# Kernel tuning notes

Measured on AMD Instinct MI355X. Metric: run time of the kernel, lower is better.

The kernel has to match this reference:

```python
import jax, jax.numpy as jnp
import numpy as np

D = 1024
H = 16
DH = D // H
FF = 4096
EPS = 1e-6


def setup_inputs() -> dict:
    key = jax.random.key(0)
    ks = jax.random.split(key, 8)
    s = 1.0 / np.sqrt(D)
    return {
        "x": jax.random.normal(ks[0], (2, 2048, D), jnp.float32),
        # attention projections stored [in, out] (math equals torch Linear x @ W.T)
        "w_q": jax.random.normal(ks[1], (D, D), jnp.float32) * s,
        "w_k": jax.random.normal(ks[2], (D, D), jnp.float32) * s,
        "w_v": jax.random.normal(ks[3], (D, D), jnp.float32) * s,
        "w_o": jax.random.normal(ks[4], (D, D), jnp.float32) * s,
        "w1": jax.random.normal(ks[5], (D, FF), jnp.float32) * s,
        "b1": jnp.zeros((FF,), jnp.float32),
        "w2": jax.random.normal(ks[6], (FF, D), jnp.float32) * (1.0 / np.sqrt(FF)),
        "b2": jnp.zeros((D,), jnp.float32),
        "g1": jnp.ones((D,), jnp.float32),
        "be1": jnp.zeros((D,), jnp.float32),
        "g2": jnp.ones((D,), jnp.float32),
        "be2": jnp.zeros((D,), jnp.float32),
    }


def _layernorm(x, gamma, beta):
    # torch .std() uses Bessel correction (ddof=1); note std+eps, not var+eps
    mean = jnp.mean(x, axis=-1, keepdims=True)
    std = jnp.std(x, axis=-1, keepdims=True, ddof=1)
    return gamma * (x - mean) / (std + EPS) + beta


def _attention(h, w_q, w_k, w_v, w_o):
    B, S, _ = h.shape
    q = (h @ w_q).reshape(B, S, H, DH)
    k = (h @ w_k).reshape(B, S, H, DH)
    v = (h @ w_v).reshape(B, S, H, DH)
    scores = jnp.einsum('bqhd,bkhd->bhqk', q, k) / np.sqrt(DH)  # [B,H,S,S]
    attn = jax.nn.softmax(scores, axis=-1)
    out = jnp.einsum('bhqk,bkhd->bqhd', attn, v).reshape(B, S, D)
    return out @ w_o


def reference(x, w_q, w_k, w_v, w_o, w1, b1, w2, b2, g1, be1, g2, be2):
    # pre-norm residual 1: self-attention (dropout=0 / eval)
    x = x + _attention(_layernorm(x, g1, be1), w_q, w_k, w_v, w_o)
    # pre-norm residual 2: FFN
    h = _layernorm(x, g2, be2)
    x = x + (jax.nn.relu(h @ w1 + b1) @ w2 + b2)
    return x
```

## Files before the change

kernel.cpp:

```cpp
#include <hip/hip_runtime.h>


typedef _Float16 half8 __attribute__((ext_vector_type(8)));
typedef _Float16 half4 __attribute__((ext_vector_type(4)));
typedef __fp16 fp16x2 __attribute__((ext_vector_type(2)));
typedef float floatx4 __attribute__((ext_vector_type(4)));

__device__ __forceinline__ void async16(const void* g, void* l) {
    __builtin_amdgcn_global_load_lds((const __attribute__((address_space(1))) unsigned int*)g,
                                     (__attribute__((address_space(3))) unsigned int*)l,
                                     16, 0, 0);
}

__global__ __launch_bounds__(256) void ln_kernel(const float* __restrict__ x,
                                                 const float* __restrict__ g,
                                                 const float* __restrict__ be,
                                                 _Float16* __restrict__ out) {
    int row = blockIdx.x;
    int tid = threadIdx.x;
    floatx4 v = ((const floatx4*)(x + (size_t)row * 1024))[tid];
    float s = 0.f, ss = 0.f;
#pragma unroll
    for (int i = 0; i < 4; i++) { s += v[i]; ss += v[i] * v[i]; }
#pragma unroll
    for (int off = 1; off < 64; off <<= 1) {
        s += __shfl_xor(s, off);
        ss += __shfl_xor(ss, off);
    }
    __shared__ float sm[8];
    int wave = tid >> 6, lane = tid & 63;
    if (lane == 0) { sm[wave] = s; sm[wave + 4] = ss; }
    __syncthreads();
    s = sm[0] + sm[1] + sm[2] + sm[3];
    ss = sm[4] + sm[5] + sm[6] + sm[7];
    float mean = s * (1.f / 1024.f);
    float var = (ss - s * mean) * (1.f / 1023.f);
    float rs = 1.f / (sqrtf(fmaxf(var, 0.f)) + 1e-6f);
    floatx4 gv = ((const floatx4*)g)[tid];
    floatx4 bv = ((const floatx4*)be)[tid];
    half4 o;
#pragma unroll
    for (int i = 0; i < 4; i++) o[i] = (_Float16)(gv[i] * (v[i] - mean) * rs + bv[i]);
    ((half4*)(out + (size_t)row * 1024))[tid] = o;
}

__global__ __launch_bounds__(256) void convt_kernel(const float* __restrict__ W, int ldW,
                                                    _Float16* __restrict__ WT, int Kr,
                                                    float scale) {
    __shared__ float t[64][65];
    int n0 = blockIdx.x * 64, k0 = blockIdx.y * 64;
    int tid = threadIdx.x;
    int r = tid >> 4, c4 = (tid & 15) * 4;
#pragma unroll
    for (int p = 0; p < 4; p++) {
        floatx4 v = *(const floatx4*)(W + (size_t)(k0 + r + p * 16) * ldW + n0 + c4);
#pragma unroll
        for (int j = 0; j < 4; j++) t[c4 + j][r + p * 16] = v[j];
    }
    __syncthreads();
#pragma unroll
    for (int p = 0; p < 4; p++) {
        int rr = r + p * 16;
        half4 o;
#pragma unroll
        for (int j = 0; j < 4; j++) o[j] = (_Float16)(t[rr][c4 + j] * scale);
        *(half4*)(WT + (size_t)(n0 + rr) * Kr + k0 + c4) = o;
    }
}

__global__ __launch_bounds__(256) void transv_kernel(const _Float16* __restrict__ V, int ldv,
                                                     _Float16* __restrict__ Vt) {
    __shared__ _Float16 t[64][72];
    int t0 = blockIdx.x * 64, d0 = blockIdx.y * 64;
    int tid = threadIdx.x;
#pragma unroll
    for (int i = 0; i < 2; i++) {
        int v = tid + i * 256;
        int r = v >> 3, c = (v & 7) * 8;
        half8 vv = *(const half8*)(V + (size_t)(t0 + r) * ldv + d0 + c);
#pragma unroll
        for (int j = 0; j < 8; j++) t[c + j][r] = vv[j];
    }
    __syncthreads();
    int bh = (t0 >> 11) * 16 + (d0 >> 6);
    int sbase = t0 & 2047;
#pragma unroll
    for (int i = 0; i < 2; i++) {
        int v = tid + i * 256;
        int r = v >> 3, c = (v & 7) * 8;
        half8 o = *(const half8*)&t[r][c];
        *(half8*)(Vt + ((size_t)bh * 64 + r) * 2048 + sbase + c) = o;
    }
}

__global__ __launch_bounds__(256) void gemm_t(const _Float16* __restrict__ A, int lda,
                                              const _Float16* __restrict__ BT,
                                              const float* __restrict__ bias,
                                              const float* res, void* Cout,
                                              int N, int K, int relu_flag, int out_fp16) {
    __shared__ _Float16 As[64 * 64];
    __shared__ _Float16 Bs[128 * 64];
    int tid = threadIdx.x;
    int wave = tid >> 6, lane = tid & 63, quad = lane >> 4, l15 = lane & 15;
    int bm = blockIdx.y * 64, bn = blockIdx.x * 128;
    int wr = (wave & 1) * 32, wc = (wave >> 1) * 64;
    int lrow = lane >> 3, lch = lane & 7;

    floatx4 acc[2][4];
#pragma unroll
    for (int im = 0; im < 2; im++)
#pragma unroll
        for (int in = 0; in < 4; in++)
#pragma unroll
            for (int r = 0; r < 4; r++) acc[im][in][r] = 0.f;

    for (int k0 = 0; k0 < K; k0 += 64) {
        __syncthreads();
#pragma unroll
        for (int ia = 0; ia < 2; ia++) {
            int g = 2 * wave + ia;
            int row = g * 8 + lrow;
            int ch = lch ^ (row & 7);
            async16(A + (size_t)(bm + row) * lda + k0 + ch * 8, &As[g * 512]);
        }
#pragma unroll
        for (int ib = 0; ib < 4; ib++) {
            int g = 4 * wave + ib;
            int row = g * 8 + lrow;
            int ch = lch ^ (row & 7);
            async16(BT + (size_t)(bn + row) * K + k0 + ch * 8, &Bs[g * 512]);
        }
        __syncthreads();

        half8 af[2][2], bf[4][2];
#pragma unroll
        for (int kk = 0; kk < 2; kk++) {
#pragma unroll
            for (int im = 0; im < 2; im++) {
                int m = wr + im * 16 + l15;
                af[im][kk] = *(const half8*)&As[m * 64 + ((((kk << 2) | quad) ^ (m & 7)) << 3)];
            }
#pragma unroll
            for (int in = 0; in < 4; in++) {
                int n = wc + in * 16 + l15;
                bf[in][kk] = *(const half8*)&Bs[n * 64 + ((((kk << 2) | quad) ^ (n & 7)) << 3)];
            }
        }
#pragma unroll
        for (int kk = 0; kk < 2; kk++)
#pragma unroll
            for (int im = 0; im < 2; im++)
#pragma unroll
                for (int in = 0; in < 4; in++)
                    acc[im][in] = __builtin_amdgcn_mfma_f32_16x16x32_f16(af[im][kk], bf[in][kk],
                                                                         acc[im][in], 0, 0, 0);
    }
#pragma unroll
    for (int im = 0; im < 2; im++)
#pragma unroll
        for (int in = 0; in < 4; in++)
#pragma unroll
            for (int r = 0; r < 4; r++) {
                int row = bm + wr + im * 16 + quad * 4 + r;
                int col = bn + wc + in * 16 + l15;
                float val = acc[im][in][r];
                if (bias) val += bias[col];
                if (relu_flag) val = fmaxf(val, 0.f);
                if (res) val += res[(size_t)row * N + col];
                if (out_fp16) ((_Float16*)Cout)[(size_t)row * N + col] = (_Float16)val;
                else          ((float*)Cout)[(size_t)row * N + col] = val;
            }
}

template <int BUF>
__device__ __forceinline__ void attn_step(const half8* const (&kfp)[2][4][2],
                                          const half4* const (&vfp)[2][4][4],
                                          const half8 (&bq)[2],
                                          floatx4 (&o_acc)[4],
                                          float& m_i, float& l_i) {
    const float LOG2E = 1.44269504f;
    floatx4 s_acc[4];
#pragma unroll
    for (int jn = 0; jn < 4; jn++)
#pragma unroll
        for (int r = 0; r < 4; r++) s_acc[jn][r] = 0.f;
#pragma unroll
    for (int jn = 0; jn < 4; jn++)
#pragma unroll
        for (int kk = 0; kk < 2; kk++)
            s_acc[jn] = __builtin_amdgcn_mfma_f32_16x16x32_f16(*kfp[BUF][jn][kk], bq[kk],
                                                               s_acc[jn], 0, 0, 0);

    float mx = -1e30f;
#pragma unroll
    for (int jn = 0; jn < 4; jn++)
#pragma unroll
        for (int r = 0; r < 4; r++) mx = fmaxf(mx, s_acc[jn][r]);
    mx = fmaxf(mx, __shfl_xor(mx, 16));
    mx = fmaxf(mx, __shfl_xor(mx, 32));
    if (!__all(mx <= m_i + 8.f)) {
        float mnew = fmaxf(m_i, mx);
        float dd = m_i - mnew;
        float alpha = (dd < -60.f) ? 0.f : __expf(dd);
        l_i *= alpha;
#pragma unroll
        for (int im = 0; im < 4; im++)
#pragma unroll
            for (int r = 0; r < 4; r++) o_acc[im][r] *= alpha;
        m_i = mnew;
    }
    float m2 = m_i * LOG2E;

    float sum = 0.f;
    half4 pb[4];
#pragma unroll
    for (int jn = 0; jn < 4; jn++) {
        float p0 = exp2f(fmaf(s_acc[jn][0], LOG2E, -m2));
        float p1 = exp2f(fmaf(s_acc[jn][1], LOG2E, -m2));
        float p2 = exp2f(fmaf(s_acc[jn][2], LOG2E, -m2));
        float p3 = exp2f(fmaf(s_acc[jn][3], LOG2E, -m2));
        sum += (p0 + p1) + (p2 + p3);
        fp16x2 lo = __builtin_amdgcn_cvt_pkrtz(p0, p1);
        fp16x2 hi = __builtin_amdgcn_cvt_pkrtz(p2, p3);
        pb[jn][0] = (_Float16)lo[0]; pb[jn][1] = (_Float16)lo[1];
        pb[jn][2] = (_Float16)hi[0]; pb[jn][3] = (_Float16)hi[1];
    }
    sum += __shfl_xor(sum, 16);
    sum += __shfl_xor(sum, 32);
    l_i += sum;

#pragma unroll
    for (int im = 0; im < 4; im++)
#pragma unroll
        for (int ks = 0; ks < 4; ks++)
            o_acc[im] = __builtin_amdgcn_mfma_f32_16x16x16f16(*vfp[BUF][im][ks], pb[ks],
                                                              o_acc[im], 0, 0, 0);
}

__global__ __launch_bounds__(256) void attn_kernel(const _Float16* Q,
                                                   const _Float16* __restrict__ K,
                                                   const _Float16* __restrict__ Vt,
                                                   _Float16* O, int ld) {
    __shared__ _Float16 Qs[64 * 64];
    __shared__ _Float16 KVs[2][2][64 * 64];
    int qt = blockIdx.x, bh = blockIdx.y;
    int b = bh >> 4, h = bh & 15;
    int col0 = h * 64, tbase = b * 2048;
    int tid = threadIdx.x;
    int wave = tid >> 6, lane = tid & 63, quad = lane >> 4, l15 = lane & 15;
    int lrow = lane >> 3, lch = lane & 7;

    const _Float16* kg[2];
    const _Float16* vg[2];
    const size_t kadv = (size_t)64 * ld;
#pragma unroll
    for (int i = 0; i < 2; i++) {
        int g = 2 * wave + i;
        int row = g * 8 + lrow;
        int ch = lch ^ (row & 7);
        kg[i] = K + (size_t)(tbase + row) * ld + col0 + ch * 8;
        vg[i] = Vt + ((size_t)bh * 64 + row) * 2048 + ch * 8;
        async16(Q + (size_t)(tbase + qt * 64 + row) * ld + col0 + ch * 8, &Qs[g * 512]);
        async16(kg[i], &KVs[0][0][g * 512]);
        async16(vg[i], &KVs[0][1][g * 512]);
        kg[i] += kadv;
        vg[i] += 64;
    }
    __syncthreads();

    int rowq = 16 * wave + l15;
    half8 bq[2];
#pragma unroll
    for (int kk = 0; kk < 2; kk++)
        bq[kk] = *(const half8*)&Qs[rowq * 64 + ((((kk << 2) | quad) ^ (rowq & 7)) << 3)];

    const half8* kfp[2][4][2];
    const half4* vfp[2][4][4];
#pragma unroll
    for (int bb = 0; bb < 2; bb++) {
#pragma unroll
        for (int jn = 0; jn < 4; jn++) {
            int rowk = 16 * jn + l15;
#pragma unroll
            for (int kk = 0; kk < 2; kk++)
                kfp[bb][jn][kk] = (const half8*)
                    &KVs[bb][0][rowk * 64 + ((((kk << 2) | quad) ^ (rowk & 7)) << 3)];
        }
#pragma unroll
        for (int im = 0; im < 4; im++) {
            int rowv = 16 * im + l15;
#pragma unroll
            for (int ks = 0; ks < 4; ks++) {
                int off = rowv * 128 + ((((2 * ks) | (quad >> 1)) ^ (rowv & 7)) << 4)
                          + (quad & 1) * 8;
                vfp[bb][im][ks] = (const half4*)((const char*)KVs[bb][1] + off);
            }
        }
    }

    floatx4 o_acc[4];
#pragma unroll
    for (int im = 0; im < 4; im++)
#pragma unroll
        for (int r = 0; r < 4; r++) o_acc[im][r] = 0.f;
    float m_i = -1e30f, l_i = 0.f;

#pragma unroll 1
    for (int kt2 = 0; kt2 < 16; kt2++) {
        if (kt2) __syncthreads();
#pragma unroll
        for (int i = 0; i < 2; i++) {
            async16(kg[i], &KVs[1][0][(2 * wave + i) * 512]);
            async16(vg[i], &KVs[1][1][(2 * wave + i) * 512]);
            kg[i] += kadv;
            vg[i] += 64;
        }
        attn_step<0>(kfp, vfp, bq, o_acc, m_i, l_i);

        __syncthreads();
        if (kt2 < 15) {
#pragma unroll
            for (int i = 0; i < 2; i++) {
                async16(kg[i], &KVs[0][0][(2 * wave + i) * 512]);
                async16(vg[i], &KVs[0][1][(2 * wave + i) * 512]);
                kg[i] += kadv;
                vg[i] += 64;
            }
        }
        attn_step<1>(kfp, vfp, bq, o_acc, m_i, l_i);
    }

    float rl = 1.f / l_i;
#pragma unroll
    for (int im = 0; im < 4; im++) {
        half4 o;
#pragma unroll
        for (int r = 0; r < 4; r++) o[r] = (_Float16)(o_acc[im][r] * rl);
        *(half4*)&O[(size_t)(tbase + qt * 64 + wave * 16 + l15) * ld + col0 + im * 16 + quad * 4] = o;
    }
}

extern "C" void kernel_launch(void* const* d_in, const int* in_sizes, int n_in,
                              void* d_out, int out_size, void* d_ws, size_t ws_size,
                              hipStream_t stream) {
    const float* x   = (const float*)d_in[0];
    const float* wq  = (const float*)d_in[1];
    const float* wk  = (const float*)d_in[2];
    const float* wv  = (const float*)d_in[3];
    const float* wo  = (const float*)d_in[4];
    const float* w1  = (const float*)d_in[5];
    const float* b1  = (const float*)d_in[6];
    const float* w2  = (const float*)d_in[7];
    const float* b2  = (const float*)d_in[8];
    const float* g1  = (const float*)d_in[9];
    const float* be1 = (const float*)d_in[10];
    const float* g2  = (const float*)d_in[11];
    const float* be2 = (const float*)d_in[12];

    const size_t M1 = (size_t)1 << 20;
    _Float16* R0  = (_Float16*)d_ws;
    _Float16* QKV = R0 + 4 * M1;
    _Float16* R3  = R0 + 12 * M1;

    _Float16* wqkvT = (_Float16*)d_out;
    float* x1 = (float*)d_out;
    float* out = (float*)d_out;

    dim3 blk(256);

    convt_kernel<<<dim3(16, 16), blk, 0, stream>>>(wq, 1024, wqkvT, 1024, 0.125f);
    convt_kernel<<<dim3(16, 16), blk, 0, stream>>>(wk, 1024, wqkvT + (size_t)1024 * 1024, 1024, 1.f);
    convt_kernel<<<dim3(16, 16), blk, 0, stream>>>(wv, 1024, wqkvT + (size_t)2048 * 1024, 1024, 1.f);
    ln_kernel<<<4096, blk, 0, stream>>>(x, g1, be1, R0);
    gemm_t<<<dim3(24, 64), blk, 0, stream>>>(R0, 1024, wqkvT, nullptr, nullptr, QKV, 3072, 1024, 0, 1);
    transv_kernel<<<dim3(64, 16), blk, 0, stream>>>(QKV + 2048, 3072, R0);
    attn_kernel<<<dim3(32, 32), blk, 0, stream>>>(QKV, QKV + 1024, R0, QKV, 3072);
    convt_kernel<<<dim3(16, 16), blk, 0, stream>>>(wo, 1024, R0, 1024, 1.f);
    gemm_t<<<dim3(8, 64), blk, 0, stream>>>(QKV, 3072, R0, nullptr, x, x1, 1024, 1024, 0, 0);
    ln_kernel<<<4096, blk, 0, stream>>>(x1, g2, be2, R0);
    _Float16* f = QKV;
    for (int hh = 0; hh < 2; hh++) {
        _Float16* w1Th = R3;
        _Float16* w2Th = R3 + 2 * M1;
        convt_kernel<<<dim3(32, 16), blk, 0, stream>>>(w1 + hh * 2048, 4096, w1Th, 1024, 1.f);
        gemm_t<<<dim3(16, 64), blk, 0, stream>>>(R0, 1024, w1Th, b1 + hh * 2048, nullptr, f,
                                                 2048, 1024, 1, 1);
        convt_kernel<<<dim3(16, 32), blk, 0, stream>>>(w2 + (size_t)hh * 2048 * 1024, 1024, w2Th, 2048, 1.f);
        gemm_t<<<dim3(8, 64), blk, 0, stream>>>(f, 2048, w2Th, (hh == 1) ? b2 : nullptr, x1, out,
                                                1024, 2048, 0, 0);
    }
}
```

Measured before the change: 465.3 us.

## Merge weight-conversion launches, add 128x128 GEMM tile for QKV, tighten softmax reductions

The three Q/K/V weight transpose-convert launches become one grid-z kernel, and each FFN half's w1/w2 conversions become one paired launch, so fewer kernels are launched. A new 128x128-tile GEMM with a 4x4 MFMA fragment per wave is used for the QKV projection to raise data reuse per block. In attention, the row-max uses a three-input max tree and the probability sum uses independent partial sums to shorten dependency chains. The larger tile uses more registers and LDS and halves the QKV grid, which may lower occupancy.

Measured after the change: 442.2 us. 1.05x faster.

```diff
diff --git a/kernel.cpp b/kernel.cpp
--- a/kernel.cpp
+++ b/kernel.cpp
@@ -5,6 +5,8 @@
 typedef _Float16 half4 __attribute__((ext_vector_type(4)));
 typedef __fp16 fp16x2 __attribute__((ext_vector_type(2)));
 typedef float floatx4 __attribute__((ext_vector_type(4)));
+
+#define MAX3(a, b, c) fmaxf(fmaxf((a), (b)), (c))
 
 __device__ __forceinline__ void async16(const void* g, void* l) {
     __builtin_amdgcn_global_load_lds((const __attribute__((address_space(1))) unsigned int*)g,
@@ -44,28 +46,60 @@
     ((half4*)(out + (size_t)row * 1024))[tid] = o;
 }
 
+__device__ __forceinline__ void convt_body(const float* __restrict__ W, int ldW,
+                                           _Float16* __restrict__ WT, int Kr, float scale,
+                                           int n0, int k0) {
+    __shared__ float t[64][65];
+    int tid = threadIdx.x;
+    int r = tid >> 4, c4 = (tid & 15) * 4;
+#pragma unroll
+    for (int p = 0; p < 4; p++) {
+        floatx4 v = *(const floatx4*)(W + (size_t)(k0 + r + p * 16) * ldW + n0 + c4);
+#pragma unroll
+        for (int j = 0; j < 4; j++) t[c4 + j][r + p * 16] = v[j];
+    }
+    __syncthreads();
+#pragma unroll
+    for (int p = 0; p < 4; p++) {
+        int rr = r + p * 16;
+        half4 o;
+#pragma unroll
+        for (int j = 0; j < 4; j++) o[j] = (_Float16)(t[rr][c4 + j] * scale);
+        *(half4*)(WT + (size_t)(n0 + rr) * Kr + k0 + c4) = o;
+    }
+}
+
 __global__ __launch_bounds__(256) void convt_kernel(const float* __restrict__ W, int ldW,
                                                     _Float16* __restrict__ WT, int Kr,
                                                     float scale) {
-    __shared__ float t[64][65];
-    int n0 = blockIdx.x * 64, k0 = blockIdx.y * 64;
-    int tid = threadIdx.x;
-    int r = tid >> 4, c4 = (tid & 15) * 4;
-#pragma unroll
-    for (int p = 0; p < 4; p++) {
-        floatx4 v = *(const floatx4*)(W + (size_t)(k0 + r + p * 16) * ldW + n0 + c4);
-#pragma unroll
-        for (int j = 0; j < 4; j++) t[c4 + j][r + p * 16] = v[j];
-    }
-    __syncthreads();
-#pragma unroll
-    for (int p = 0; p < 4; p++) {
-        int rr = r + p * 16;
-        half4 o;
-#pragma unroll
-        for (int j = 0; j < 4; j++) o[j] = (_Float16)(t[rr][c4 + j] * scale);
-        *(half4*)(WT + (size_t)(n0 + rr) * Kr + k0 + c4) = o;
-    }
+    convt_body(W, ldW, WT, Kr, scale, blockIdx.x * 64, blockIdx.y * 64);
+}
+
+__global__ __launch_bounds__(256) void convt3_kernel(const float* __restrict__ W0,
+                                                     const float* __restrict__ W1,
+                                                     const float* __restrict__ W2,
+                                                     _Float16* __restrict__ QT) {
+    int z = blockIdx.z;
+    const float* W = (z == 0) ? W0 : (z == 1) ? W1 : W2;
+    _Float16* WT = QT + (size_t)z * 1024 * 1024;
+    float scale = (z == 0) ? 0.125f : 1.f;
+    convt_body(W, 1024, WT, 1024, scale, blockIdx.x * 64, blockIdx.y * 64);
+}
+
+__global__ __launch_bounds__(256) void convt_pair_kernel(const float* __restrict__ Wa, int ldWa,
+                                                         _Float16* __restrict__ WTa, int Kra,
+                                                         int gxa, int gya,
+                                                         const float* __restrict__ Wb, int ldWb,
+                                                         _Float16* __restrict__ WTb, int Krb,
+                                                         int gxb, int gyb) {
+    int z = blockIdx.z;
+    const float* W = z ? Wb : Wa;
+    _Float16* WT = z ? WTb : WTa;
+    int ldW = z ? ldWb : ldWa;
+    int Kr = z ? Krb : Kra;
+    int gx = z ? gxb : gxa, gy = z ? gyb : gya;
+    if ((int)blockIdx.x >= gx || (int)blockIdx.y >= gy) return;
+    convt_body(W, ldW, WT, Kr, 1.f, blockIdx.x * 64, blockIdx.y * 64);
 }
 
 __global__ __launch_bounds__(256) void transv_kernel(const _Float16* __restrict__ V, int ldv,
@@ -172,6 +206,85 @@
             }
 }
 
+__global__ __launch_bounds__(256) void gemm_t128(const _Float16* __restrict__ A, int lda,
+                                                 const _Float16* __restrict__ BT,
+                                                 const float* __restrict__ bias,
+                                                 const float* res, void* Cout,
+                                                 int N, int K, int relu_flag, int out_fp16) {
+    __shared__ _Float16 As[128 * 64];
+    __shared__ _Float16 Bs[128 * 64];
+    int tid = threadIdx.x;
+    int wave = tid >> 6, lane = tid & 63, quad = lane >> 4, l15 = lane & 15;
+    int bm = blockIdx.y * 128, bn = blockIdx.x * 128;
+    int wr = (wave & 1) * 64, wc = (wave >> 1) * 64;
+    int lrow = lane >> 3, lch = lane & 7;
+
+    floatx4 acc[4][4];
+#pragma unroll
+    for (int im = 0; im < 4; im++)
+#pragma unroll
+        for (int in = 0; in < 4; in++)
+#pragma unroll
+            for (int r = 0; r < 4; r++) acc[im][in][r] = 0.f;
+
+    for (int k0 = 0; k0 < K; k0 += 64) {
+        __syncthreads();
+#pragma unroll
+        for (int ia = 0; ia < 4; ia++) {
+            int g = 4 * wave + ia;
+            int row = g * 8 + lrow;
+            int ch = lch ^ (row & 7);
+            async16(A + (size_t)(bm + row) * lda + k0 + ch * 8, &As[g * 512]);
+        }
+#pragma unroll
+        for (int ib = 0; ib < 4; ib++) {
+            int g = 4 * wave + ib;
+            int row = g * 8 + lrow;
+            int ch = lch ^ (row & 7);
+            async16(BT + (size_t)(bn + row) * K + k0 + ch * 8, &Bs[g * 512]);
+        }
+        __syncthreads();
+
+        half8 af[4][2], bf[4][2];
+#pragma unroll
+        for (int kk = 0; kk < 2; kk++) {
+#pragma unroll
+            for (int im = 0; im < 4; im++) {
+                int m = wr + im * 16 + l15;
+                af[im][kk] = *(const half8*)&As[m * 64 + ((((kk << 2) | quad) ^ (m & 7)) << 3)];
+            }
+#pragma unroll
+            for (int in = 0; in < 4; in++) {
+                int n = wc + in * 16 + l15;
+                bf[in][kk] = *(const half8*)&Bs[n * 64 + ((((kk << 2) | quad) ^ (n & 7)) << 3)];
+            }
+        }
+#pragma unroll
+        for (int kk = 0; kk < 2; kk++)
+#pragma unroll
+            for (int im = 0; im < 4; im++)
+#pragma unroll
+                for (int in = 0; in < 4; in++)
+                    acc[im][in] = __builtin_amdgcn_mfma_f32_16x16x32_f16(af[im][kk], bf[in][kk],
+                                                                         acc[im][in], 0, 0, 0);
+    }
+#pragma unroll
+    for (int im = 0; im < 4; im++)
+#pragma unroll
+        for (int in = 0; in < 4; in++)
+#pragma unroll
+            for (int r = 0; r < 4; r++) {
+                int row = bm + wr + im * 16 + quad * 4 + r;
+                int col = bn + wc + in * 16 + l15;
+                float val = acc[im][in][r];
+                if (bias) val += bias[col];
+                if (relu_flag) val = fmaxf(val, 0.f);
+                if (res) val += res[(size_t)row * N + col];
+                if (out_fp16) ((_Float16*)Cout)[(size_t)row * N + col] = (_Float16)val;
+                else          ((float*)Cout)[(size_t)row * N + col] = val;
+            }
+}
+
 template <int BUF>
 __device__ __forceinline__ void attn_step(const half8* const (&kfp)[2][4][2],
                                           const half4* const (&vfp)[2][4][4],
@@ -191,11 +304,12 @@
             s_acc[jn] = __builtin_amdgcn_mfma_f32_16x16x32_f16(*kfp[BUF][jn][kk], bq[kk],
                                                                s_acc[jn], 0, 0, 0);
 
-    float mx = -1e30f;
-#pragma unroll
-    for (int jn = 0; jn < 4; jn++)
-#pragma unroll
-        for (int r = 0; r < 4; r++) mx = fmaxf(mx, s_acc[jn][r]);
+    float t0 = MAX3(s_acc[0][0], s_acc[0][1], s_acc[0][2]);
+    float t1 = MAX3(s_acc[0][3], s_acc[1][0], s_acc[1][1]);
+    float t2 = MAX3(s_acc[1][2], s_acc[1][3], s_acc[2][0]);
+    float t3 = MAX3(s_acc[2][1], s_acc[2][2], s_acc[2][3]);
+    float t4 = MAX3(s_acc[3][0], s_acc[3][1], s_acc[3][2]);
+    float mx = MAX3(MAX3(t0, t1, t2), fmaxf(t3, t4), s_acc[3][3]);
     mx = fmaxf(mx, __shfl_xor(mx, 16));
     mx = fmaxf(mx, __shfl_xor(mx, 32));
     if (!__all(mx <= m_i + 8.f)) {
@@ -211,7 +325,7 @@
     }
     float m2 = m_i * LOG2E;
 
-    float sum = 0.f;
+    float sj[4];
     half4 pb[4];
 #pragma unroll
     for (int jn = 0; jn < 4; jn++) {
@@ -219,12 +333,13 @@
         float p1 = exp2f(fmaf(s_acc[jn][1], LOG2E, -m2));
         float p2 = exp2f(fmaf(s_acc[jn][2], LOG2E, -m2));
         float p3 = exp2f(fmaf(s_acc[jn][3], LOG2E, -m2));
-        sum += (p0 + p1) + (p2 + p3);
+        sj[jn] = (p0 + p1) + (p2 + p3);
         fp16x2 lo = __builtin_amdgcn_cvt_pkrtz(p0, p1);
         fp16x2 hi = __builtin_amdgcn_cvt_pkrtz(p2, p3);
         pb[jn][0] = (_Float16)lo[0]; pb[jn][1] = (_Float16)lo[1];
         pb[jn][2] = (_Float16)hi[0]; pb[jn][3] = (_Float16)hi[1];
     }
+    float sum = (sj[0] + sj[1]) + (sj[2] + sj[3]);
     sum += __shfl_xor(sum, 16);
     sum += __shfl_xor(sum, 32);
     l_i += sum;
@@ -368,24 +483,24 @@
 
     dim3 blk(256);
 
-    convt_kernel<<<dim3(16, 16), blk, 0, stream>>>(wq, 1024, wqkvT, 1024, 0.125f);
-    convt_kernel<<<dim3(16, 16), blk, 0, stream>>>(wk, 1024, wqkvT + (size_t)1024 * 1024, 1024, 1.f);
-    convt_kernel<<<dim3(16, 16), blk, 0, stream>>>(wv, 1024, wqkvT + (size_t)2048 * 1024, 1024, 1.f);
+    convt3_kernel<<<dim3(16, 16, 3), blk, 0, stream>>>(wq, wk, wv, wqkvT);
     ln_kernel<<<4096, blk, 0, stream>>>(x, g1, be1, R0);
-    gemm_t<<<dim3(24, 64), blk, 0, stream>>>(R0, 1024, wqkvT, nullptr, nullptr, QKV, 3072, 1024, 0, 1);
+    gemm_t128<<<dim3(24, 32), blk, 0, stream>>>(R0, 1024, wqkvT, nullptr, nullptr, QKV, 3072, 1024, 0, 1);
     transv_kernel<<<dim3(64, 16), blk, 0, stream>>>(QKV + 2048, 3072, R0);
     attn_kernel<<<dim3(32, 32), blk, 0, stream>>>(QKV, QKV + 1024, R0, QKV, 3072);
-    convt_kernel<<<dim3(16, 16), blk, 0, stream>>>(wo, 1024, R0, 1024, 1.f);
-    gemm_t<<<dim3(8, 64), blk, 0, stream>>>(QKV, 3072, R0, nullptr, x, x1, 1024, 1024, 0, 0);
+    _Float16* woT = R0;
+    convt_kernel<<<dim3(16, 16), blk, 0, stream>>>(wo, 1024, woT, 1024, 1.f);
+    gemm_t<<<dim3(8, 64), blk, 0, stream>>>(QKV, 3072, woT, nullptr, x, x1, 1024, 1024, 0, 0);
     ln_kernel<<<4096, blk, 0, stream>>>(x1, g2, be2, R0);
     _Float16* f = QKV;
     for (int hh = 0; hh < 2; hh++) {
         _Float16* w1Th = R3;
         _Float16* w2Th = R3 + 2 * M1;
-        convt_kernel<<<dim3(32, 16), blk, 0, stream>>>(w1 + hh * 2048, 4096, w1Th, 1024, 1.f);
+        convt_pair_kernel<<<dim3(32, 32, 2), blk, 0, stream>>>(
+            w1 + hh * 2048, 4096, w1Th, 1024, 32, 16,
+            w2 + (size_t)hh * 2048 * 1024, 1024, w2Th, 2048, 16, 32);
         gemm_t<<<dim3(16, 64), blk, 0, stream>>>(R0, 1024, w1Th, b1 + hh * 2048, nullptr, f,
                                                  2048, 1024, 1, 1);
-        convt_kernel<<<dim3(16, 32), blk, 0, stream>>>(w2 + (size_t)hh * 2048 * 1024, 1024, w2Th, 2048, 1.f);
         gemm_t<<<dim3(8, 64), blk, 0, stream>>>(f, 2048, w2Th, (hh == 1) ? b2 : nullptr, x1, out,
                                                 1024, 2048, 0, 0);
     }
```
